# Performance work log

Measured on AMD Instinct MI355X. Metric: run time of the kernel, lower is better.

The kernel has to match this reference:

```python
import jax, jax.numpy as jnp
import numpy as np

ALPHA = 0.5


def _chamfer(a, b):
    # Equivalent math to cKDTree k=1 queries: exact nearest-neighbor distances
    # between the two flattened clouds, computed brute-force.
    a = a.reshape(-1, 3)
    b = b.reshape(-1, 3)
    d2 = (jnp.sum(a * a, axis=1)[:, None]
          + jnp.sum(b * b, axis=1)[None, :]
          - 2.0 * (a @ b.T))                      # [Na, Nb]
    d = jnp.sqrt(jnp.clip(d2, 0.0))
    dist1 = jnp.min(d, axis=0)   # tree1(a).query(b): NN dist of each b point
    dist2 = jnp.min(d, axis=1)   # tree2(b).query(a): NN dist of each a point
    return jnp.mean(dist1) + jnp.mean(dist2)


def _pairwise_distances(x, y):
    # x: [B,N,3], y: [B,M,3] -> [B,N,M] euclidean distances (clamped-sqrt trick)
    x2 = jnp.sum(x * x, axis=-1, keepdims=True)            # [B,N,1]
    y2 = jnp.sum(y * y, axis=-1, keepdims=True)            # [B,M,1]
    d2 = x2 + jnp.swapaxes(y2, 2, 1) - 2.0 * jnp.einsum('bnd,bmd->bnm', x, y)
    return jnp.sqrt(jnp.clip(d2, 0.0))


def _confidence_scores(input_pcd, gt_pcd):
    # Faithful to torch.norm on the broadcast difference: [B,P,M,3] -> [B,P,M]
    diff = input_pcd[:, :, None, :] - gt_pcd[:, None, :, :]
    dist = jnp.linalg.norm(diff, axis=-1)
    min_d = jnp.min(dist, axis=-1)                         # [B,P]
    return jnp.exp(-min_d)[..., None]                      # [B,P,1]


def setup_inputs() -> dict:
    key = jax.random.key(0)
    k0, k1, k2, k3, k4 = jax.random.split(key, 5)
    B, N, M, P, NS = 4, 2048, 2048, 2048, 1024
    return {
        'pc1_0': jax.random.normal(k0, (B, N, 3), dtype=jnp.float32),
        'pc1_1': jax.random.normal(k1, (B, NS, 3), dtype=jnp.float32),
        'pc1_3': jax.random.uniform(k2, (B, P, 1), dtype=jnp.float32),
        'pc2': jax.random.normal(k3, (B, M, 3), dtype=jnp.float32),
        'pc3': jax.random.normal(k4, (B, P, 3), dtype=jnp.float32),
    }


def reference(pc1_0, pc1_1, pc1_3, pc2, pc3):
    # ChamferDistance detaches inputs in torch (cpu/numpy path) -> stop_gradient
    cd = jax.lax.stop_gradient(_chamfer(pc1_0, pc2))
    # In the original, emd_dist is immediately overwritten by pairwise_distances
    emd_dist = _pairwise_distances(pc1_0, pc2)             # [B,N,M]
    gt_scores = _confidence_scores(pc3, pc2)               # [B,P,1]
    confidence_loss = jnp.mean((pc1_3 - gt_scores) ** 2)
    seed_loss = jax.lax.stop_gradient(_chamfer(pc1_1, pc2))
    upsampling_loss = ALPHA * cd + (1.0 - ALPHA) * emd_dist
    final_loss = confidence_loss + upsampling_loss + seed_loss  # broadcasts to [B,N,M]
    return final_loss
```

## Files before the change

### kernel.cpp

```cpp
#include <hip/hip_runtime.h>
#include <math.h>


constexpr int GMIN_TOTAL = 36864;
constexpr int OUT_TOTAL  = 4 * 2048 * 2048;
constexpr int GMIN_OFS   = OUT_TOTAL - GMIN_TOTAL;

__global__ __launch_bounds__(256) void init_min(unsigned int* __restrict__ g,
                                                float* __restrict__ ws) {
    int blk = blockIdx.x;
    if (blk == 144) { if (threadIdx.x < 8) ws[threadIdx.x] = 0.f; return; }
    int i = blk * 256 + threadIdx.x;
    g[i] = 0x7F800000u;
}

__global__ __launch_bounds__(256) void nn_kernel(
    const float* __restrict__ A0,
    const float* __restrict__ A1,
    const float* __restrict__ P2,
    const float* __restrict__ P3,
    float* __restrict__ gmin)
{
    __shared__ float4 lds[256];
    int bid = blockIdx.x;
    const float* A; const float* Bp; int b_tiles; int gofs; int local;
    if (bid < 256)      { local = bid;       A = A0; Bp = P2; b_tiles = 32; gofs = 0; }
    else if (bid < 512) { local = bid - 256; A = P2; Bp = A0; b_tiles = 32; gofs = 8192; }
    else if (bid < 640) { local = bid - 512; A = A1; Bp = P2; b_tiles = 32; gofs = 16384; }
    else if (bid < 768) { local = bid - 640; A = P2; Bp = A1; b_tiles = 16; gofs = 20480; }
    else { int l2 = bid - 768; int bt = l2 >> 4; local = l2 & 15;
           A = P3 + bt * 6144; Bp = P2 + bt * 6144; b_tiles = 8; gofs = 28672 + bt * 2048; }
    int a_tile = local / b_tiles;
    int b_tile = local - a_tile * b_tiles;

    {
        const float* s = Bp + (b_tile * 256 + threadIdx.x) * 3;
        float bx = s[0], by = s[1], bz = s[2];
        float hb2 = 0.5f * fmaf(bx, bx, fmaf(by, by, bz * bz));
        lds[threadIdx.x] = make_float4(bx, by, bz, hb2);
    }

    int a_base = a_tile * 1024 + threadIdx.x * 4;
    const float4* av = (const float4*)(A + a_base * 3);
    float4 v0 = av[0], v1 = av[1], v2 = av[2];
    float ax[4], ay[4], az[4], a2[4], mn[4];
    ax[0]=v0.x; ay[0]=v0.y; az[0]=v0.z;
    ax[1]=v0.w; ay[1]=v1.x; az[1]=v1.y;
    ax[2]=v1.z; ay[2]=v1.w; az[2]=v2.x;
    ax[3]=v2.y; ay[3]=v2.z; az[3]=v2.w;
    #pragma unroll
    for (int k = 0; k < 4; k++) {
        a2[k] = fmaf(ax[k], ax[k], fmaf(ay[k], ay[k], az[k]*az[k]));
        mn[k] = 3.4e38f;
    }
    __syncthreads();

    #pragma unroll 4
    for (int j = 0; j < 256; j++) {
        float4 b = lds[j];
        #pragma unroll
        for (int k = 0; k < 4; k++) {
            float t = fmaf(ax[k], b.x, fmaf(ay[k], b.y, az[k]*b.z));
            mn[k] = fminf(mn[k], b.w - t);
        }
    }
    #pragma unroll
    for (int k = 0; k < 4; k++) {
        float d2 = fmaxf(fmaf(2.f, mn[k], a2[k]), 0.f);
        atomicMin((unsigned int*)(gmin + gofs + a_base + k), __float_as_uint(d2));
    }
}

__global__ __launch_bounds__(256) void reduce_kernel(
    const float* __restrict__ gmin,
    const float* __restrict__ conf_in,
    float* __restrict__ ws)
{
    int blk = blockIdx.x;
    int tid = threadIdx.x;
    int base = blk * 1024;
    float sum = 0.f;
    if (blk < 28) {
        #pragma unroll
        for (int r = 0; r < 4; r++) sum += sqrtf(gmin[base + tid + r * 256]);
    } else {
        int cbase = base - 28672;
        #pragma unroll
        for (int r = 0; r < 4; r++) {
            int i = tid + r * 256;
            float d = sqrtf(gmin[base + i]);
            float e = conf_in[cbase + i] - __expf(-d);
            sum += e * e;
        }
    }
    #pragma unroll
    for (int ofs = 32; ofs > 0; ofs >>= 1) sum += __shfl_down(sum, ofs);
    __shared__ float red[4];
    int wave = tid >> 6;
    if ((tid & 63) == 0) red[wave] = sum;
    __syncthreads();
    if (tid == 0) {
        float tot = red[0] + red[1] + red[2] + red[3];
        float scale = (blk < 16) ? 0.5f / 8192.f
                    : (blk < 20) ? 1.f / 4096.f
                    :              1.f / 8192.f;
        atomicAdd(&ws[1], tot * scale);
    }
}

__global__ __launch_bounds__(256) void out_kernel(
    const float* __restrict__ pc1_0,
    const float* __restrict__ pc2,
    const float* __restrict__ Sp,
    float* __restrict__ out)
{
    int blk = blockIdx.x;
    int batch = blk >> 8;
    int n8 = blk & 255;
    int tid = threadIdx.x;
    float S = Sp[1];
    const float* bb = pc2 + batch * 6144;
    float bx[8], by[8], bz[8];
    {
        const float4* p = (const float4*)(bb + tid * 12);
        float4 u0 = p[0], u1 = p[1], u2 = p[2];
        bx[0]=u0.x; by[0]=u0.y; bz[0]=u0.z;
        bx[1]=u0.w; by[1]=u1.x; bz[1]=u1.y;
        bx[2]=u1.z; by[2]=u1.w; bz[2]=u2.x;
        bx[3]=u2.y; by[3]=u2.z; bz[3]=u2.w;
    }
    {
        const float4* p = (const float4*)(bb + 3072 + tid * 12);
        float4 u0 = p[0], u1 = p[1], u2 = p[2];
        bx[4]=u0.x; by[4]=u0.y; bz[4]=u0.z;
        bx[5]=u0.w; by[5]=u1.x; bz[5]=u1.y;
        bx[6]=u1.z; by[6]=u1.w; bz[6]=u2.x;
        bx[7]=u2.y; by[7]=u2.z; bz[7]=u2.w;
    }
    const float* arow = pc1_0 + batch * 6144 + n8 * 24;
    float* ob = out + (long)((batch << 11) + (n8 << 3)) * 2048 + tid * 4;
    #pragma unroll
    for (int r = 0; r < 8; r++) {
        float axx = arow[r*3], ayy = arow[r*3+1], azz = arow[r*3+2];
        float o[8];
        #pragma unroll
        for (int k = 0; k < 8; k++) {
            float dx = axx - bx[k], dy = ayy - by[k], dz = azz - bz[k];
            float d2 = fmaf(dx, dx, fmaf(dy, dy, dz*dz));
            o[k] = fmaf(0.5f, sqrtf(d2), S);
        }
        *(float4*)(ob + r * 2048)        = make_float4(o[0], o[1], o[2], o[3]);
        *(float4*)(ob + r * 2048 + 1024) = make_float4(o[4], o[5], o[6], o[7]);
    }
}

extern "C" void kernel_launch(void* const* d_in, const int* in_sizes, int n_in,
                              void* d_out, int out_size, void* d_ws, size_t ws_size,
                              hipStream_t stream) {
    const float* pc1_0 = (const float*)d_in[0];
    const float* pc1_1 = (const float*)d_in[1];
    const float* pc1_3 = (const float*)d_in[2];
    const float* pc2   = (const float*)d_in[3];
    const float* pc3   = (const float*)d_in[4];
    float* out = (float*)d_out;
    float* ws  = (float*)d_ws;
    float* gmin = out + GMIN_OFS;

    init_min<<<145, 256, 0, stream>>>((unsigned int*)gmin, ws);
    nn_kernel<<<832, 256, 0, stream>>>(pc1_0, pc1_1, pc2, pc3, gmin);
    reduce_kernel<<<36, 256, 0, stream>>>(gmin, pc1_3, ws);
    out_kernel<<<1024, 256, 0, stream>>>(pc1_0, pc2, ws, out);
}
```

Before: 114.4 us.

## Replace atomic min/add with per-block partials and deterministic two-stage reduction

```diff
diff --git a/kernel.cpp b/kernel.cpp
--- a/kernel.cpp
+++ b/kernel.cpp
@@ -2,48 +2,42 @@
 #include <math.h>
 
 
-constexpr int GMIN_TOTAL = 36864;
 constexpr int OUT_TOTAL  = 4 * 2048 * 2048;
-constexpr int GMIN_OFS   = OUT_TOTAL - GMIN_TOTAL;
+constexpr int PART_TOTAL = 832 * 1024;
+constexpr int PART_OFS   = OUT_TOTAL - PART_TOTAL;
 
-__global__ __launch_bounds__(256) void init_min(unsigned int* __restrict__ g,
-                                                float* __restrict__ ws) {
-    int blk = blockIdx.x;
-    if (blk == 144) { if (threadIdx.x < 8) ws[threadIdx.x] = 0.f; return; }
-    int i = blk * 256 + threadIdx.x;
-    g[i] = 0x7F800000u;
-}
+typedef float nfloat4 __attribute__((ext_vector_type(4)));
 
 __global__ __launch_bounds__(256) void nn_kernel(
     const float* __restrict__ A0,
     const float* __restrict__ A1,
     const float* __restrict__ P2,
     const float* __restrict__ P3,
-    float* __restrict__ gmin)
+    float* __restrict__ part)
 {
     __shared__ float4 lds[256];
     int bid = blockIdx.x;
-    const float* A; const float* Bp; int b_tiles; int gofs; int local;
-    if (bid < 256)      { local = bid;       A = A0; Bp = P2; b_tiles = 32; gofs = 0; }
-    else if (bid < 512) { local = bid - 256; A = P2; Bp = A0; b_tiles = 32; gofs = 8192; }
-    else if (bid < 640) { local = bid - 512; A = A1; Bp = P2; b_tiles = 32; gofs = 16384; }
-    else if (bid < 768) { local = bid - 640; A = P2; Bp = A1; b_tiles = 16; gofs = 20480; }
+    const float* A; const float* Bp; int b_tiles; int local;
+    if (bid < 256)      { local = bid;       A = A0; Bp = P2; b_tiles = 32; }
+    else if (bid < 512) { local = bid - 256; A = P2; Bp = A0; b_tiles = 32; }
+    else if (bid < 640) { local = bid - 512; A = A1; Bp = P2; b_tiles = 32; }
+    else if (bid < 768) { local = bid - 640; A = P2; Bp = A1; b_tiles = 16; }
     else { int l2 = bid - 768; int bt = l2 >> 4; local = l2 & 15;
-           A = P3 + bt * 6144; Bp = P2 + bt * 6144; b_tiles = 8; gofs = 28672 + bt * 2048; }
+           A = P3 + bt * 6144; Bp = P2 + bt * 6144; b_tiles = 8; }
     int a_tile = local / b_tiles;
     int b_tile = local - a_tile * b_tiles;
 
     {
         const float* s = Bp + (b_tile * 256 + threadIdx.x) * 3;
         float bx = s[0], by = s[1], bz = s[2];
-        float hb2 = 0.5f * fmaf(bx, bx, fmaf(by, by, bz * bz));
-        lds[threadIdx.x] = make_float4(bx, by, bz, hb2);
+        float nb2 = -0.5f * fmaf(bx, bx, fmaf(by, by, bz * bz));
+        lds[threadIdx.x] = make_float4(bx, by, bz, nb2);
     }
 
     int a_base = a_tile * 1024 + threadIdx.x * 4;
     const float4* av = (const float4*)(A + a_base * 3);
     float4 v0 = av[0], v1 = av[1], v2 = av[2];
-    float ax[4], ay[4], az[4], a2[4], mn[4];
+    float ax[4], ay[4], az[4], a2[4], mx[4];
     ax[0]=v0.x; ay[0]=v0.y; az[0]=v0.z;
     ax[1]=v0.w; ay[1]=v1.x; az[1]=v1.y;
     ax[2]=v1.z; ay[2]=v1.w; az[2]=v2.x;
@@ -51,7 +45,7 @@
     #pragma unroll
     for (int k = 0; k < 4; k++) {
         a2[k] = fmaf(ax[k], ax[k], fmaf(ay[k], ay[k], az[k]*az[k]));
-        mn[k] = 3.4e38f;
+        mx[k] = -3.4e38f;
     }
     __syncthreads();
 
@@ -60,65 +54,82 @@
         float4 b = lds[j];
         #pragma unroll
         for (int k = 0; k < 4; k++) {
-            float t = fmaf(ax[k], b.x, fmaf(ay[k], b.y, az[k]*b.z));
-            mn[k] = fminf(mn[k], b.w - t);
+            float u = fmaf(az[k], b.z, b.w);
+            u = fmaf(ay[k], b.y, u);
+            u = fmaf(ax[k], b.x, u);
+            mx[k] = fmaxf(mx[k], u);
         }
     }
-    #pragma unroll
-    for (int k = 0; k < 4; k++) {
-        float d2 = fmaxf(fmaf(2.f, mn[k], a2[k]), 0.f);
-        atomicMin((unsigned int*)(gmin + gofs + a_base + k), __float_as_uint(d2));
-    }
+    float4 o;
+    o.x = fmaxf(fmaf(-2.f, mx[0], a2[0]), 0.f);
+    o.y = fmaxf(fmaf(-2.f, mx[1], a2[1]), 0.f);
+    o.z = fmaxf(fmaf(-2.f, mx[2], a2[2]), 0.f);
+    o.w = fmaxf(fmaf(-2.f, mx[3], a2[3]), 0.f);
+    *(float4*)(part + bid * 1024 + threadIdx.x * 4) = o;
 }
 
 __global__ __launch_bounds__(256) void reduce_kernel(
-    const float* __restrict__ gmin,
+    const float* __restrict__ part,
     const float* __restrict__ conf_in,
     float* __restrict__ ws)
 {
     int blk = blockIdx.x;
     int tid = threadIdx.x;
-    int base = blk * 1024;
-    float sum = 0.f;
+    int pb, bt;
+    if (blk < 8)       { pb = blk * 32;              bt = 32; }
+    else if (blk < 16) { pb = 256 + (blk - 8) * 32;  bt = 32; }
+    else if (blk < 20) { pb = 512 + (blk - 16) * 32; bt = 32; }
+    else if (blk < 28) { pb = 640 + (blk - 20) * 16; bt = 16; }
+    else               { pb = 768 + (blk - 28) * 8;  bt = 8;  }
+
+    float m0 = 3.4e38f, m1 = 3.4e38f, m2 = 3.4e38f, m3 = 3.4e38f;
+    const float* p = part + (pb << 10) + tid;
+    #pragma unroll 4
+    for (int t = 0; t < bt; t++, p += 1024) {
+        m0 = fminf(m0, p[0]);
+        m1 = fminf(m1, p[256]);
+        m2 = fminf(m2, p[512]);
+        m3 = fminf(m3, p[768]);
+    }
+    float d0 = sqrtf(m0), d1 = sqrtf(m1), d2 = sqrtf(m2), d3 = sqrtf(m3);
+    float sum;
     if (blk < 28) {
-        #pragma unroll
-        for (int r = 0; r < 4; r++) sum += sqrtf(gmin[base + tid + r * 256]);
+        sum = (d0 + d1) + (d2 + d3);
     } else {
-        int cbase = base - 28672;
-        #pragma unroll
-        for (int r = 0; r < 4; r++) {
-            int i = tid + r * 256;
-            float d = sqrtf(gmin[base + i]);
-            float e = conf_in[cbase + i] - __expf(-d);
-            sum += e * e;
-        }
+        const float* c = conf_in + (blk - 28) * 1024 + tid;
+        float e0 = c[0]   - __expf(-d0);
+        float e1 = c[256] - __expf(-d1);
+        float e2 = c[512] - __expf(-d2);
+        float e3 = c[768] - __expf(-d3);
+        sum = fmaf(e0, e0, e1 * e1) + fmaf(e2, e2, e3 * e3);
     }
     #pragma unroll
     for (int ofs = 32; ofs > 0; ofs >>= 1) sum += __shfl_down(sum, ofs);
     __shared__ float red[4];
-    int wave = tid >> 6;
-    if ((tid & 63) == 0) red[wave] = sum;
+    if ((tid & 63) == 0) red[tid >> 6] = sum;
     __syncthreads();
     if (tid == 0) {
-        float tot = red[0] + red[1] + red[2] + red[3];
+        float tot = (red[0] + red[1]) + (red[2] + red[3]);
         float scale = (blk < 16) ? 0.5f / 8192.f
                     : (blk < 20) ? 1.f / 4096.f
                     :              1.f / 8192.f;
-        atomicAdd(&ws[1], tot * scale);
+        ws[blk] = tot * scale;
     }
 }
 
 __global__ __launch_bounds__(256) void out_kernel(
     const float* __restrict__ pc1_0,
     const float* __restrict__ pc2,
-    const float* __restrict__ Sp,
+    const float* __restrict__ wsp,
     float* __restrict__ out)
 {
     int blk = blockIdx.x;
     int batch = blk >> 8;
     int n8 = blk & 255;
     int tid = threadIdx.x;
-    float S = Sp[1];
+    float S = 0.f;
+    #pragma unroll
+    for (int t = 0; t < 36; t++) S += wsp[t];
     const float* bb = pc2 + batch * 6144;
     float bx[8], by[8], bz[8];
     {
@@ -149,8 +160,10 @@
             float d2 = fmaf(dx, dx, fmaf(dy, dy, dz*dz));
             o[k] = fmaf(0.5f, sqrtf(d2), S);
         }
-        *(float4*)(ob + r * 2048)        = make_float4(o[0], o[1], o[2], o[3]);
-        *(float4*)(ob + r * 2048 + 1024) = make_float4(o[4], o[5], o[6], o[7]);
+        nfloat4 lo = { o[0], o[1], o[2], o[3] };
+        nfloat4 hi = { o[4], o[5], o[6], o[7] };
+        __builtin_nontemporal_store(lo, (nfloat4*)(ob + r * 2048));
+        __builtin_nontemporal_store(hi, (nfloat4*)(ob + r * 2048 + 1024));
     }
 }
 
@@ -164,10 +177,9 @@
     const float* pc3   = (const float*)d_in[4];
     float* out = (float*)d_out;
     float* ws  = (float*)d_ws;
-    float* gmin = out + GMIN_OFS;
+    float* part = out + PART_OFS;
 
-    init_min<<<145, 256, 0, stream>>>((unsigned int*)gmin, ws);
-    nn_kernel<<<832, 256, 0, stream>>>(pc1_0, pc1_1, pc2, pc3, gmin);
-    reduce_kernel<<<36, 256, 0, stream>>>(gmin, pc1_3, ws);
+    nn_kernel<<<832, 256, 0, stream>>>(pc1_0, pc1_1, pc2, pc3, part);
+    reduce_kernel<<<36, 256, 0, stream>>>(part, pc1_3, ws);
     out_kernel<<<1024, 256, 0, stream>>>(pc1_0, pc2, ws, out);
 }
```

Result: faster. 111.5 us (-2.5%).
